# Performance work log

Hardware: AMD Instinct MI355X
Metric: run time of the kernel (lower is better)

Reference implementation:

```python
import jax, jax.numpy as jnp
import numpy as np

K = 2  # top-k experts per token

def setup_inputs() -> dict:
    key = jax.random.key(0)
    ks = jax.random.split(key, 8)
    B, S, D, F, E = 2, 1024, 1024, 4096, 8
    s_in = 1.0 / np.sqrt(D)
    s_mid = 1.0 / np.sqrt(F)
    return {
        "x": jax.random.normal(ks[0], (B, S, D), dtype=jnp.float32),
        "Wr": jax.random.uniform(ks[1], (D, E), jnp.float32, -s_in, s_in),
        "br": jax.random.uniform(ks[2], (E,), jnp.float32, -s_in, s_in),
        "W1": jax.random.uniform(ks[3], (E, D, F), jnp.float32, -s_in, s_in),
        "b1": jax.random.uniform(ks[4], (E, F), jnp.float32, -s_in, s_in),
        "W2": jax.random.uniform(ks[5], (E, F, D), jnp.float32, -s_mid, s_mid),
        "b2": jax.random.uniform(ks[6], (E, D), jnp.float32, -s_mid, s_mid),
    }

def _moe(x, Wr, br, W1, b1, W2, b2):
    E = Wr.shape[1]
    # router (eval mode: no noise)
    logits = jnp.einsum('bsd,de->bse', x, Wr) + br          # [B,S,E]
    topk_logits, topk_idx = jax.lax.top_k(logits, K)        # [B,S,K]
    router_probs = jax.nn.softmax(topk_logits, axis=-1)     # [B,S,K]
    # per-expert combine weight: sum over k slots assigned to expert e
    onehot = jax.nn.one_hot(topk_idx, E, dtype=x.dtype)     # [B,S,K,E]
    w = jnp.einsum('bske,bsk->bse', onehot, router_probs)   # [B,S,E]
    # scan over experts (fixed small E), accumulate weighted expert outputs
    def step(acc, ew):
        W1j, b1j, W2j, b2j, wj = ew                          # wj: [B,S]
        h = jax.nn.gelu(jnp.einsum('bsd,df->bsf', x, W1j) + b1j, approximate=False)
        y = jnp.einsum('bsf,fd->bsd', h, W2j) + b2j
        return acc + y * wj[..., None], None
    out, _ = jax.lax.scan(step, jnp.zeros_like(x),
                          (W1, b1, W2, b2, jnp.transpose(w, (2, 0, 1))))
    return out, router_probs

def reference(x, Wr, br, W1, b1, W2, b2):
    return _moe(x, Wr, br, W1, b1, W2, b2)
```

## Files before the change

kernel.cpp:

```cpp
#include <hip/hip_runtime.h>
#include <hip/hip_bf16.h>
#include <cstdint>

#define TOKENS 2048
#define Dm 1024
#define Fm 4096
#define Em 8

typedef short s16x8 __attribute__((ext_vector_type(8)));
typedef float f32x4 __attribute__((ext_vector_type(4)));

#define GLOAD16(g, l) __builtin_amdgcn_global_load_lds(                     \
    (const __attribute__((address_space(1))) void*)(g),                     \
    (__attribute__((address_space(3))) void*)(l), 16, 0, 0)

__device__ __forceinline__ ushort f2bf(float f) {
  union { float f; uint32_t u; } v; v.f = f;
  uint32_t r = v.u + 0x7fffu + ((v.u >> 16) & 1u);
  return (ushort)(r >> 16);
}

__global__ void transcvt(const float* __restrict__ in, ushort* __restrict__ out,
                         int R, int C) {
  __shared__ float tile[32][33];
  int e = blockIdx.z;
  const float* src = in + (size_t)e * R * C;
  ushort* dst = out + (size_t)e * R * C;
  int c0 = blockIdx.x * 32, r0 = blockIdx.y * 32;
  int lr = threadIdx.x >> 5, lc = threadIdx.x & 31;
#pragma unroll
  for (int p = 0; p < 4; ++p) {
    int r = r0 + p * 8 + lr;
    tile[p * 8 + lr][lc] = src[(size_t)r * C + c0 + lc];
  }
  __syncthreads();
#pragma unroll
  for (int p = 0; p < 4; ++p) {
    int c = c0 + p * 8 + lr;
    dst[(size_t)c * R + r0 + lc] = f2bf(tile[lc][p * 8 + lr]);
  }
}

__global__ void router(const float* __restrict__ x, const float* __restrict__ Wr,
                       const float* __restrict__ br, float* __restrict__ probs,
                       int* __restrict__ e_sel, float* __restrict__ w_sel,
                       ushort* __restrict__ xb) {
  int t = blockIdx.x;
  const float4* xr4 = (const float4*)(x + (size_t)t * Dm);
  float4 v = xr4[threadIdx.x];
  ushort4 o;
  o.x = f2bf(v.x); o.y = f2bf(v.y); o.z = f2bf(v.z); o.w = f2bf(v.w);
  ((ushort4*)(xb + (size_t)t * Dm))[threadIdx.x] = o;

  int d0 = threadIdx.x * 4;
  const float4* wr4 = (const float4*)(Wr + (size_t)d0 * Em);
  float wv[4][8];
#pragma unroll
  for (int r = 0; r < 4; ++r) {
    float4 a = wr4[r * 2], b = wr4[r * 2 + 1];
    wv[r][0] = a.x; wv[r][1] = a.y; wv[r][2] = a.z; wv[r][3] = a.w;
    wv[r][4] = b.x; wv[r][5] = b.y; wv[r][6] = b.z; wv[r][7] = b.w;
  }
  float xs[4] = {v.x, v.y, v.z, v.w};
  float acc[Em];
#pragma unroll
  for (int e = 0; e < Em; ++e)
    acc[e] = xs[0] * wv[0][e] + xs[1] * wv[1][e] + xs[2] * wv[2][e] + xs[3] * wv[3][e];

#pragma unroll
  for (int off = 32; off >= 1; off >>= 1)
#pragma unroll
    for (int e = 0; e < Em; ++e) acc[e] += __shfl_down(acc[e], off);
  __shared__ float red[4][Em];
  int lane = threadIdx.x & 63, wid = threadIdx.x >> 6;
  if (lane == 0)
#pragma unroll
    for (int e = 0; e < Em; ++e) red[wid][e] = acc[e];
  __syncthreads();
  if (threadIdx.x == 0) {
    float lg[Em];
#pragma unroll
    for (int e = 0; e < Em; ++e)
      lg[e] = red[0][e] + red[1][e] + red[2][e] + red[3][e] + br[e];
    int i0 = 0;
    for (int e = 1; e < Em; ++e) if (lg[e] > lg[i0]) i0 = e;
    int i1 = -1;
    for (int e = 0; e < Em; ++e) {
      if (e == i0) continue;
      if (i1 < 0 || lg[e] > lg[i1]) i1 = e;
    }
    float d = lg[i1] - lg[i0];
    float tt = expf(d);
    float inv = 1.f / (1.f + tt);
    float p0 = inv, p1 = tt * inv;
    probs[t * 2] = p0; probs[t * 2 + 1] = p1;
    e_sel[t * 2] = i0; e_sel[t * 2 + 1] = i1;
    w_sel[t * 2] = p0; w_sel[t * 2 + 1] = p1;
  }
}

__global__ void build_lists(const int* __restrict__ e_sel, const float* __restrict__ w_sel,
                            int* __restrict__ tok_of_row, float* __restrict__ w_of_row,
                            int* __restrict__ base, int* __restrict__ npad,
                            int* __restrict__ ncnt) {
  __shared__ int cnt[Em], run[Em], sbase[Em];
  __shared__ int wsum[4][Em];
  int tid = threadIdx.x, lane = tid & 63, wid = tid >> 6;
  if (tid < Em) { cnt[tid] = 0; run[tid] = 0; }
  __syncthreads();
  for (int t = tid; t < TOKENS; t += 256) {
    atomicAdd(&cnt[e_sel[2 * t]], 1);
    atomicAdd(&cnt[e_sel[2 * t + 1]], 1);
  }
  __syncthreads();
  if (tid == 0) {
    int b = 0;
    for (int e = 0; e < Em; ++e) {
      base[e] = b; sbase[e] = b;
      int n = cnt[e]; ncnt[e] = n;
      int p = (n + 127) & ~127;
      npad[e] = p; b += p;
    }
  }
  __syncthreads();
  for (int c = 0; c < TOKENS / 256; ++c) {
    int t = c * 256 + tid;
    int e0 = e_sel[2 * t], e1 = e_sel[2 * t + 1];
    unsigned long long mm[Em];
#pragma unroll
    for (int e = 0; e < Em; ++e) {
      unsigned long long m0 = __ballot(e0 == e);
      unsigned long long m1 = __ballot(e1 == e);
      mm[e] = m0 | m1;
      if (lane == 0) wsum[wid][e] = __popcll(mm[e]);
    }
    __syncthreads();
    unsigned long long below = (1ull << lane) - 1ull;
    {
      int e = e0;
      int p = __popcll(mm[e] & below);
      int pre = 0;
      for (int w = 0; w < wid; ++w) pre += wsum[w][e];
      int row = sbase[e] + run[e] + pre + p;
      tok_of_row[row] = t; w_of_row[row] = w_sel[2 * t];
    }
    {
      int e = e1;
      int p = __popcll(mm[e] & below);
      int pre = 0;
      for (int w = 0; w < wid; ++w) pre += wsum[w][e];
      int row = sbase[e] + run[e] + pre + p;
      tok_of_row[row] = t; w_of_row[row] = w_sel[2 * t + 1];
    }
    __syncthreads();
    if (tid < Em) {
      int s = 0;
      for (int w = 0; w < 4; ++w) s += wsum[w][tid];
      run[tid] += s;
    }
    __syncthreads();
  }
  for (int e = 0; e < Em; ++e) {
    int n = cnt[e];
    int p = (n + 127) & ~127;
    for (int i = n + tid; i < p; i += 256) {
      tok_of_row[sbase[e] + i] = -1;
      w_of_row[sbase[e] + i] = 0.f;
    }
  }
}

__global__ void out_init(const int* __restrict__ e_sel, const float* __restrict__ w_sel,
                         const float* __restrict__ b2, float* __restrict__ out) {
  int t = blockIdx.x;
  int e0 = e_sel[2 * t], e1 = e_sel[2 * t + 1];
  float w0 = w_sel[2 * t], w1 = w_sel[2 * t + 1];
  const float4* p0 = (const float4*)(b2 + (size_t)e0 * Dm);
  const float4* p1 = (const float4*)(b2 + (size_t)e1 * Dm);
  float4* o = (float4*)(out + (size_t)t * Dm);
  for (int i = threadIdx.x; i < Dm / 4; i += 256) {
    float4 a = p0[i], b = p1[i];
    float4 r;
    r.x = w0 * a.x + w1 * b.x; r.y = w0 * a.y + w1 * b.y;
    r.z = w0 * a.z + w1 * b.z; r.w = w0 * a.w + w1 * b.w;
    o[i] = r;
  }
}

__global__ __launch_bounds__(256) void gemm1(
    const ushort* __restrict__ xb, const ushort* __restrict__ bmat,
    const float* __restrict__ b1, ushort* __restrict__ H,
    const int* __restrict__ tok_of_row, const int* __restrict__ base,
    const int* __restrict__ npad) {
  int e = blockIdx.y >> 4, rt = blockIdx.y & 15;
  int np = npad[e];
  if (rt * 128 >= np) return;
  int row0 = base[e] + rt * 128;
  int n0 = blockIdx.x * 128;
  __shared__ ushort As[128 * 32];
  __shared__ ushort Bs[128 * 32];
  __shared__ int toks[128];
  int tid = threadIdx.x, lane = tid & 63, wid = tid >> 6;
  if (tid < 128) toks[tid] = tok_of_row[row0 + tid];
  __syncthreads();
  int arow = tid >> 2, asub = tid & 3;
  int t0 = toks[arow];      if (t0 < 0) t0 = 0;
  int t1 = toks[64 + arow]; if (t1 < 0) t1 = 0;
  const ushort* sA0 = xb + (size_t)t0 * Dm + asub * 8;
  const ushort* sA1 = xb + (size_t)t1 * Dm + asub * 8;
  const ushort* sB0 = bmat + ((size_t)e * Fm + n0 + arow) * Dm + asub * 8;
  const ushort* sB1 = sB0 + (size_t)64 * Dm;
  char* ldA0 = (char*)As + wid * 1024;
  char* ldA1 = (char*)As + 4096 + wid * 1024;
  char* ldB0 = (char*)Bs + wid * 1024;
  char* ldB1 = (char*)Bs + 4096 + wid * 1024;
  int wr = wid >> 1, wc = wid & 1;
  const ushort* aB = As + ((size_t)(wr * 64 + (lane & 15)) * 32) + (lane >> 4) * 8;
  const ushort* bB = Bs + ((size_t)(wc * 64 + (lane & 15)) * 32) + (lane >> 4) * 8;
  f32x4 acc[4][4] = {};
  for (int kt = 0; kt < Dm / 32; ++kt) {
    GLOAD16(sA0, ldA0);
    GLOAD16(sA1, ldA1);
    GLOAD16(sB0, ldB0);
    GLOAD16(sB1, ldB1);
    sA0 += 32; sA1 += 32; sB0 += 32; sB1 += 32;
    __syncthreads();
    s16x8 av[4], bv[4];
#pragma unroll
    for (int m = 0; m < 4; ++m) av[m] = *(const s16x8*)(aB + m * 512);
#pragma unroll
    for (int n = 0; n < 4; ++n) bv[n] = *(const s16x8*)(bB + n * 512);
#pragma unroll
    for (int m = 0; m < 4; ++m)
#pragma unroll
      for (int n = 0; n < 4; ++n)
        acc[m][n] = __builtin_amdgcn_mfma_f32_16x16x32_bf16(av[m], bv[n], acc[m][n], 0, 0, 0);
    __syncthreads();
  }
  int rb = wr * 64 + ((lane >> 4) << 2);
  int cb = n0 + wc * 64 + (lane & 15);
#pragma unroll
  for (int n = 0; n < 4; ++n) {
    int col = cb + n * 16;
    float bias = b1[e * Fm + col];
#pragma unroll
    for (int m = 0; m < 4; ++m) {
      int r = row0 + rb + m * 16;
#pragma unroll
      for (int j = 0; j < 4; ++j) {
        float v = acc[m][n][j] + bias;
        float g = 0.5f * v * (1.f + erff(v * 0.70710678118654752f));
        H[(size_t)(r + j) * Fm + col] = f2bf(g);
      }
    }
  }
}

__global__ __launch_bounds__(256) void gemm2(
    const ushort* __restrict__ H, const ushort* __restrict__ bmat,
    const int* __restrict__ tok_of_row, const float* __restrict__ w_of_row,
    const int* __restrict__ base, const int* __restrict__ npad,
    float* __restrict__ out) {
  int e = blockIdx.y >> 4, rt = blockIdx.y & 15;
  int np = npad[e];
  if (rt * 128 >= np) return;
  int row0 = base[e] + rt * 128;
  int n0 = blockIdx.x * 128;
  int k0 = blockIdx.z * (Fm / 2);
  __shared__ ushort As[128 * 32];
  __shared__ ushort Bs[128 * 32];
  __shared__ int toks[128];
  __shared__ float wts[128];
  int tid = threadIdx.x, lane = tid & 63, wid = tid >> 6;
  if (tid < 128) {
    toks[tid] = tok_of_row[row0 + tid];
    wts[tid] = w_of_row[row0 + tid];
  }
  __syncthreads();
  int arow = tid >> 2, asub = tid & 3;
  const ushort* sA0 = H + (size_t)(row0 + arow) * Fm + k0 + asub * 8;
  const ushort* sA1 = sA0 + (size_t)64 * Fm;
  const ushort* sB0 = bmat + ((size_t)e * Dm + n0 + arow) * Fm + k0 + asub * 8;
  const ushort* sB1 = sB0 + (size_t)64 * Fm;
  char* ldA0 = (char*)As + wid * 1024;
  char* ldA1 = (char*)As + 4096 + wid * 1024;
  char* ldB0 = (char*)Bs + wid * 1024;
  char* ldB1 = (char*)Bs + 4096 + wid * 1024;
  int wr = wid >> 1, wc = wid & 1;
  const ushort* aB = As + ((size_t)(wr * 64 + (lane & 15)) * 32) + (lane >> 4) * 8;
  const ushort* bB = Bs + ((size_t)(wc * 64 + (lane & 15)) * 32) + (lane >> 4) * 8;
  f32x4 acc[4][4] = {};
  for (int kt = 0; kt < Fm / 2 / 32; ++kt) {
    GLOAD16(sA0, ldA0);
    GLOAD16(sA1, ldA1);
    GLOAD16(sB0, ldB0);
    GLOAD16(sB1, ldB1);
    sA0 += 32; sA1 += 32; sB0 += 32; sB1 += 32;
    __syncthreads();
    s16x8 av[4], bv[4];
#pragma unroll
    for (int m = 0; m < 4; ++m) av[m] = *(const s16x8*)(aB + m * 512);
#pragma unroll
    for (int n = 0; n < 4; ++n) bv[n] = *(const s16x8*)(bB + n * 512);
#pragma unroll
    for (int m = 0; m < 4; ++m)
#pragma unroll
      for (int n = 0; n < 4; ++n)
        acc[m][n] = __builtin_amdgcn_mfma_f32_16x16x32_bf16(av[m], bv[n], acc[m][n], 0, 0, 0);
    __syncthreads();
  }
  int rb = wr * 64 + ((lane >> 4) << 2);
  int cb = n0 + wc * 64 + (lane & 15);
#pragma unroll
  for (int n = 0; n < 4; ++n) {
    int col = cb + n * 16;
#pragma unroll
    for (int m = 0; m < 4; ++m) {
      int rl = rb + m * 16;
#pragma unroll
      for (int j = 0; j < 4; ++j) {
        int tok = toks[rl + j];
        if (tok >= 0)
          atomicAdd(&out[(size_t)tok * Dm + col], wts[rl + j] * acc[m][n][j]);
      }
    }
  }
}

extern "C" void kernel_launch(void* const* d_in, const int* in_sizes, int n_in,
                              void* d_out, int out_size, void* d_ws, size_t ws_size,
                              hipStream_t stream) {
  const float* x  = (const float*)d_in[0];
  const float* Wr = (const float*)d_in[1];
  const float* br = (const float*)d_in[2];
  const float* W1 = (const float*)d_in[3];
  const float* b1 = (const float*)d_in[4];
  const float* W2 = (const float*)d_in[5];
  const float* b2 = (const float*)d_in[6];
  float* out = (float*)d_out;
  float* probs = out + (size_t)TOKENS * Dm;

  char* ws = (char*)d_ws;
  ushort* Wt   = (ushort*)ws;
  ushort* Hbuf = (ushort*)(ws + 67108864);
  ushort* xb   = (ushort*)(ws + 109051904);
  int*   tok_of_row = (int*)(ws + 113246208);
  float* w_of_row   = (float*)(ws + 113266688);
  int*   e_sel      = (int*)(ws + 113287168);
  float* w_sel      = (float*)(ws + 113303552);
  int*   meta       = (int*)(ws + 113319936);

  transcvt<<<dim3(Fm / 32, Dm / 32, Em), 256, 0, stream>>>(W1, Wt, Dm, Fm);
  router<<<TOKENS, 256, 0, stream>>>(x, Wr, br, probs, e_sel, w_sel, xb);
  build_lists<<<1, 256, 0, stream>>>(e_sel, w_sel, tok_of_row, w_of_row,
                                     meta, meta + 8, meta + 16);
  out_init<<<TOKENS, 256, 0, stream>>>(e_sel, w_sel, b2, out);
  gemm1<<<dim3(32, 128), 256, 0, stream>>>(xb, Wt, b1, Hbuf, tok_of_row,
                                           meta, meta + 8);
  transcvt<<<dim3(Dm / 32, Fm / 32, Em), 256, 0, stream>>>(W2, Wt, Fm, Dm);
  gemm2<<<dim3(8, 128, 2), 256, 0, stream>>>(Hbuf, Wt, tok_of_row, w_of_row,
                                             meta, meta + 8, out);
}
```

Baseline: 275.7 us.

## Fuse weight transposes with router into one prep kernel, fold b2 into gemm2

Merges the W1 (and W2, when the workspace is large enough) transpose-convert and the router into a single launch. It replaces the out_init kernel with a memset plus a bias term added in gemm2's first K-split. It also doubles gemm2's split-K from 2 to 4 for more parallelism. The trade-offs are more atomic adds to the output, and behaviour that depends on workspace size.

```diff
diff --git a/kernel.cpp b/kernel.cpp
--- a/kernel.cpp
+++ b/kernel.cpp
@@ -22,66 +22,94 @@
 
 __global__ void transcvt(const float* __restrict__ in, ushort* __restrict__ out,
                          int R, int C) {
-  __shared__ float tile[32][33];
+  __shared__ float tile[32 * 33];
   int e = blockIdx.z;
   const float* src = in + (size_t)e * R * C;
   ushort* dst = out + (size_t)e * R * C;
   int c0 = blockIdx.x * 32, r0 = blockIdx.y * 32;
   int lr = threadIdx.x >> 5, lc = threadIdx.x & 31;
 #pragma unroll
-  for (int p = 0; p < 4; ++p) {
-    int r = r0 + p * 8 + lr;
-    tile[p * 8 + lr][lc] = src[(size_t)r * C + c0 + lc];
-  }
-  __syncthreads();
-#pragma unroll
-  for (int p = 0; p < 4; ++p) {
-    int c = c0 + p * 8 + lr;
-    dst[(size_t)c * R + r0 + lc] = f2bf(tile[lc][p * 8 + lr]);
-  }
-}
-
-__global__ void router(const float* __restrict__ x, const float* __restrict__ Wr,
-                       const float* __restrict__ br, float* __restrict__ probs,
-                       int* __restrict__ e_sel, float* __restrict__ w_sel,
-                       ushort* __restrict__ xb) {
-  int t = blockIdx.x;
+  for (int p = 0; p < 4; ++p)
+    tile[(p * 8 + lr) * 33 + lc] = src[(size_t)(r0 + p * 8 + lr) * C + c0 + lc];
+  __syncthreads();
+#pragma unroll
+  for (int p = 0; p < 4; ++p)
+    dst[(size_t)(c0 + p * 8 + lr) * R + r0 + lc] = f2bf(tile[lc * 33 + p * 8 + lr]);
+}
+
+__global__ void prep(const float* __restrict__ W1, ushort* __restrict__ W1T,
+                     const float* __restrict__ W2, ushort* __restrict__ W2T,
+                     int do_w2,
+                     const float* __restrict__ x, const float* __restrict__ Wr,
+                     const float* __restrict__ br, float* __restrict__ probs,
+                     int* __restrict__ e_sel, float* __restrict__ w_sel,
+                     ushort* __restrict__ xb) {
+  __shared__ float shf[32 * 33];
+  int b = blockIdx.x;
+  if (b < 65536) {
+    const float* src;
+    ushort* dst;
+    size_t sstride, dstride;
+    if (b < 32768) {
+      int cx = b & 127, ry = (b >> 7) & 31, e = b >> 12;
+      src = W1 + ((size_t)e * Dm + ry * 32) * Fm + cx * 32;
+      dst = W1T + ((size_t)e * Fm + cx * 32) * Dm + ry * 32;
+      sstride = Fm; dstride = Dm;
+    } else {
+      if (!do_w2) return;
+      int b2i = b - 32768;
+      int cx = b2i & 31, ry = (b2i >> 5) & 127, e = b2i >> 12;
+      src = W2 + ((size_t)e * Fm + ry * 32) * Dm + cx * 32;
+      dst = W2T + ((size_t)e * Dm + cx * 32) * Fm + ry * 32;
+      sstride = Dm; dstride = Fm;
+    }
+    int lr = threadIdx.x >> 5, lc = threadIdx.x & 31;
+#pragma unroll
+    for (int p = 0; p < 4; ++p)
+      shf[(p * 8 + lr) * 33 + lc] = src[(size_t)(p * 8 + lr) * sstride + lc];
+    __syncthreads();
+#pragma unroll
+    for (int p = 0; p < 4; ++p)
+      dst[(size_t)(p * 8 + lr) * dstride + lc] = f2bf(shf[lc * 33 + p * 8 + lr]);
+    return;
+  }
+  int t = b - 65536;
+  int tid = threadIdx.x;
   const float4* xr4 = (const float4*)(x + (size_t)t * Dm);
-  float4 v = xr4[threadIdx.x];
+  float4 v = xr4[tid];
   ushort4 o;
   o.x = f2bf(v.x); o.y = f2bf(v.y); o.z = f2bf(v.z); o.w = f2bf(v.w);
-  ((ushort4*)(xb + (size_t)t * Dm))[threadIdx.x] = o;
-
-  int d0 = threadIdx.x * 4;
+  ((ushort4*)(xb + (size_t)t * Dm))[tid] = o;
+
+  int d0 = tid * 4;
   const float4* wr4 = (const float4*)(Wr + (size_t)d0 * Em);
   float wv[4][8];
 #pragma unroll
   for (int r = 0; r < 4; ++r) {
-    float4 a = wr4[r * 2], b = wr4[r * 2 + 1];
+    float4 a = wr4[r * 2], bq = wr4[r * 2 + 1];
     wv[r][0] = a.x; wv[r][1] = a.y; wv[r][2] = a.z; wv[r][3] = a.w;
-    wv[r][4] = b.x; wv[r][5] = b.y; wv[r][6] = b.z; wv[r][7] = b.w;
+    wv[r][4] = bq.x; wv[r][5] = bq.y; wv[r][6] = bq.z; wv[r][7] = bq.w;
   }
   float xs[4] = {v.x, v.y, v.z, v.w};
   float acc[Em];
 #pragma unroll
   for (int e = 0; e < Em; ++e)
     acc[e] = xs[0] * wv[0][e] + xs[1] * wv[1][e] + xs[2] * wv[2][e] + xs[3] * wv[3][e];
-
 #pragma unroll
   for (int off = 32; off >= 1; off >>= 1)
 #pragma unroll
     for (int e = 0; e < Em; ++e) acc[e] += __shfl_down(acc[e], off);
-  __shared__ float red[4][Em];
-  int lane = threadIdx.x & 63, wid = threadIdx.x >> 6;
+  float* red = shf;
+  int lane = tid & 63, wid = tid >> 6;
   if (lane == 0)
 #pragma unroll
-    for (int e = 0; e < Em; ++e) red[wid][e] = acc[e];
-  __syncthreads();
-  if (threadIdx.x == 0) {
+    for (int e = 0; e < Em; ++e) red[wid * 8 + e] = acc[e];
+  __syncthreads();
+  if (tid == 0) {
     float lg[Em];
 #pragma unroll
     for (int e = 0; e < Em; ++e)
-      lg[e] = red[0][e] + red[1][e] + red[2][e] + red[3][e] + br[e];
+      lg[e] = red[e] + red[8 + e] + red[16 + e] + red[24 + e] + br[e];
     int i0 = 0;
     for (int e = 1; e < Em; ++e) if (lg[e] > lg[i0]) i0 = e;
     int i1 = -1;
@@ -92,17 +120,15 @@
     float d = lg[i1] - lg[i0];
     float tt = expf(d);
     float inv = 1.f / (1.f + tt);
-    float p0 = inv, p1 = tt * inv;
-    probs[t * 2] = p0; probs[t * 2 + 1] = p1;
+    probs[t * 2] = inv; probs[t * 2 + 1] = tt * inv;
     e_sel[t * 2] = i0; e_sel[t * 2 + 1] = i1;
-    w_sel[t * 2] = p0; w_sel[t * 2 + 1] = p1;
+    w_sel[t * 2] = inv; w_sel[t * 2 + 1] = tt * inv;
   }
 }
 
 __global__ void build_lists(const int* __restrict__ e_sel, const float* __restrict__ w_sel,
                             int* __restrict__ tok_of_row, float* __restrict__ w_of_row,
-                            int* __restrict__ base, int* __restrict__ npad,
-                            int* __restrict__ ncnt) {
+                            int* __restrict__ base, int* __restrict__ npad) {
   __shared__ int cnt[Em], run[Em], sbase[Em];
   __shared__ int wsum[4][Em];
   int tid = threadIdx.x, lane = tid & 63, wid = tid >> 6;
@@ -117,7 +143,7 @@
     int b = 0;
     for (int e = 0; e < Em; ++e) {
       base[e] = b; sbase[e] = b;
-      int n = cnt[e]; ncnt[e] = n;
+      int n = cnt[e];
       int p = (n + 127) & ~127;
       npad[e] = p; b += p;
     }
@@ -170,25 +196,8 @@
   }
 }
 
-__global__ void out_init(const int* __restrict__ e_sel, const float* __restrict__ w_sel,
-                         const float* __restrict__ b2, float* __restrict__ out) {
-  int t = blockIdx.x;
-  int e0 = e_sel[2 * t], e1 = e_sel[2 * t + 1];
-  float w0 = w_sel[2 * t], w1 = w_sel[2 * t + 1];
-  const float4* p0 = (const float4*)(b2 + (size_t)e0 * Dm);
-  const float4* p1 = (const float4*)(b2 + (size_t)e1 * Dm);
-  float4* o = (float4*)(out + (size_t)t * Dm);
-  for (int i = threadIdx.x; i < Dm / 4; i += 256) {
-    float4 a = p0[i], b = p1[i];
-    float4 r;
-    r.x = w0 * a.x + w1 * b.x; r.y = w0 * a.y + w1 * b.y;
-    r.z = w0 * a.z + w1 * b.z; r.w = w0 * a.w + w1 * b.w;
-    o[i] = r;
-  }
-}
-
 __global__ __launch_bounds__(256) void gemm1(
-    const ushort* __restrict__ xb, const ushort* __restrict__ bmat,
+    const ushort* __restrict__ xb, const ushort* __restrict__ W1T,
     const float* __restrict__ b1, ushort* __restrict__ H,
     const int* __restrict__ tok_of_row, const int* __restrict__ base,
     const int* __restrict__ npad) {
@@ -208,7 +217,7 @@
   int t1 = toks[64 + arow]; if (t1 < 0) t1 = 0;
   const ushort* sA0 = xb + (size_t)t0 * Dm + asub * 8;
   const ushort* sA1 = xb + (size_t)t1 * Dm + asub * 8;
-  const ushort* sB0 = bmat + ((size_t)e * Fm + n0 + arow) * Dm + asub * 8;
+  const ushort* sB0 = W1T + ((size_t)e * Fm + n0 + arow) * Dm + asub * 8;
   const ushort* sB1 = sB0 + (size_t)64 * Dm;
   char* ldA0 = (char*)As + wid * 1024;
   char* ldA1 = (char*)As + 4096 + wid * 1024;
@@ -257,7 +266,8 @@
 }
 
 __global__ __launch_bounds__(256) void gemm2(
-    const ushort* __restrict__ H, const ushort* __restrict__ bmat,
+    const ushort* __restrict__ H, const ushort* __restrict__ W2T,
+    const float* __restrict__ b2,
     const int* __restrict__ tok_of_row, const float* __restrict__ w_of_row,
     const int* __restrict__ base, const int* __restrict__ npad,
     float* __restrict__ out) {
@@ -266,7 +276,7 @@
   if (rt * 128 >= np) return;
   int row0 = base[e] + rt * 128;
   int n0 = blockIdx.x * 128;
-  int k0 = blockIdx.z * (Fm / 2);
+  int k0 = blockIdx.z * (Fm / 4);
   __shared__ ushort As[128 * 32];
   __shared__ ushort Bs[128 * 32];
   __shared__ int toks[128];
@@ -280,7 +290,7 @@
   int arow = tid >> 2, asub = tid & 3;
   const ushort* sA0 = H + (size_t)(row0 + arow) * Fm + k0 + asub * 8;
   const ushort* sA1 = sA0 + (size_t)64 * Fm;
-  const ushort* sB0 = bmat + ((size_t)e * Dm + n0 + arow) * Fm + k0 + asub * 8;
+  const ushort* sB0 = W2T + ((size_t)e * Dm + n0 + arow) * Fm + k0 + asub * 8;
   const ushort* sB1 = sB0 + (size_t)64 * Fm;
   char* ldA0 = (char*)As + wid * 1024;
   char* ldA1 = (char*)As + 4096 + wid * 1024;
@@ -290,7 +300,7 @@
   const ushort* aB = As + ((size_t)(wr * 64 + (lane & 15)) * 32) + (lane >> 4) * 8;
   const ushort* bB = Bs + ((size_t)(wc * 64 + (lane & 15)) * 32) + (lane >> 4) * 8;
   f32x4 acc[4][4] = {};
-  for (int kt = 0; kt < Fm / 2 / 32; ++kt) {
+  for (int kt = 0; kt < Fm / 4 / 32; ++kt) {
     GLOAD16(sA0, ldA0);
     GLOAD16(sA1, ldA1);
     GLOAD16(sB0, ldB0);
@@ -311,9 +321,11 @@
   }
   int rb = wr * 64 + ((lane >> 4) << 2);
   int cb = n0 + wc * 64 + (lane & 15);
+  int add_bias = (blockIdx.z == 0);
 #pragma unroll
   for (int n = 0; n < 4; ++n) {
     int col = cb + n * 16;
+    float bias = add_bias ? b2[e * Dm + col] : 0.f;
 #pragma unroll
     for (int m = 0; m < 4; ++m) {
       int rl = rb + m * 16;
@@ -321,7 +333,7 @@
       for (int j = 0; j < 4; ++j) {
         int tok = toks[rl + j];
         if (tok >= 0)
-          atomicAdd(&out[(size_t)tok * Dm + col], wts[rl + j] * acc[m][n][j]);
+          atomicAdd(&out[(size_t)tok * Dm + col], wts[rl + j] * (acc[m][n][j] + bias));
       }
     }
   }
@@ -341,7 +353,7 @@
   float* probs = out + (size_t)TOKENS * Dm;
 
   char* ws = (char*)d_ws;
-  ushort* Wt   = (ushort*)ws;
+  ushort* W1T  = (ushort*)ws;
   ushort* Hbuf = (ushort*)(ws + 67108864);
   ushort* xb   = (ushort*)(ws + 109051904);
   int*   tok_of_row = (int*)(ws + 113246208);
@@ -349,15 +361,18 @@
   int*   e_sel      = (int*)(ws + 113287168);
   float* w_sel      = (float*)(ws + 113303552);
   int*   meta       = (int*)(ws + 113319936);
-
-  transcvt<<<dim3(Fm / 32, Dm / 32, Em), 256, 0, stream>>>(W1, Wt, Dm, Fm);
-  router<<<TOKENS, 256, 0, stream>>>(x, Wr, br, probs, e_sel, w_sel, xb);
+  int sep = (ws_size >= 180429056ULL) ? 1 : 0;
+  ushort* W2T = sep ? (ushort*)(ws + 113320192) : W1T;
+
+  hipMemsetAsync(out, 0, (size_t)TOKENS * Dm * sizeof(float), stream);
+  prep<<<65536 + TOKENS, 256, 0, stream>>>(W1, W1T, W2, W2T, sep, x, Wr, br,
+                                           probs, e_sel, w_sel, xb);
   build_lists<<<1, 256, 0, stream>>>(e_sel, w_sel, tok_of_row, w_of_row,
-                                     meta, meta + 8, meta + 16);
-  out_init<<<TOKENS, 256, 0, stream>>>(e_sel, w_sel, b2, out);
-  gemm1<<<dim3(32, 128), 256, 0, stream>>>(xb, Wt, b1, Hbuf, tok_of_row,
+                                     meta, meta + 8);
+  gemm1<<<dim3(32, 128), 256, 0, stream>>>(xb, W1T, b1, Hbuf, tok_of_row,
                                            meta, meta + 8);
-  transcvt<<<dim3(Dm / 32, Fm / 32, Em), 256, 0, stream>>>(W2, Wt, Fm, Dm);
-  gemm2<<<dim3(8, 128, 2), 256, 0, stream>>>(Hbuf, Wt, tok_of_row, w_of_row,
+  if (!sep)
+    transcvt<<<dim3(Dm / 32, Fm / 32, Em), 256, 0, stream>>>(W2, W2T, Fm, Dm);
+  gemm2<<<dim3(8, 128, 4), 256, 0, stream>>>(Hbuf, W2T, b2, tok_of_row, w_of_row,
                                              meta, meta + 8, out);
 }
```

Measured after the change: 323.7 us. +17.4%, slower.
